# Kernel tuning notes

Measured on AMD Instinct MI355X. Metric: run time of the kernel, lower is better.

The kernel has to match this reference:

```python
import jax, jax.numpy as jnp
import numpy as np

# Hyperparameters (from init_kwargs)
N = 100000      # num_nodes
T = 4           # num_edge_type
E = 400000      # edges per type
C = 2           # num_channels
L = 2           # num_layers
W_IN = 128      # input feature dim
D = 64          # node_dim (w_out)
NUM_CLASS = 16
BETA = 0.5
M = 10000       # number of target nodes


def setup_inputs() -> dict:
    key = jax.random.key(0)
    ks = jax.random.split(key, 10)
    glorot = np.sqrt(6.0 / (W_IN + D))
    glorot1 = np.sqrt(6.0 / (C * D + D))
    glorot2 = np.sqrt(6.0 / (D + NUM_CLASS))
    return {
        "X": jax.random.normal(ks[0], (N, W_IN), dtype=jnp.float32),
        "edge_value": jax.random.uniform(ks[1], (T, E), dtype=jnp.float32),
        "conv_weights": 0.1 * jax.random.normal(ks[2], (L, C, T), dtype=jnp.float32),
        "Ws": jax.random.uniform(ks[3], (C, W_IN, D), minval=-glorot, maxval=glorot, dtype=jnp.float32),
        "lin1_w": jax.random.uniform(ks[4], (C * D, D), minval=-glorot1, maxval=glorot1, dtype=jnp.float32),
        "lin1_b": jnp.zeros((D,), dtype=jnp.float32),
        "lin_w": jax.random.uniform(ks[5], (D, NUM_CLASS), minval=-glorot2, maxval=glorot2, dtype=jnp.float32),
        "lin_b": jnp.zeros((NUM_CLASS,), dtype=jnp.float32),
        "edge_index": jax.random.randint(ks[6], (T, 2, E), 0, N),
        "target_x": jax.random.randint(ks[7], (M,), 0, N),
    }


def reference(X, edge_value, conv_weights, Ws, lin1_w, lin1_b, lin_w, lin_b,
              edge_index, target_x):
    # Flatten edge types into one big edge list. torch_sparse.coalesce(op='add')
    # followed by torch.sparse.mm is mathematically a duplicate-summing SpMM,
    # i.e. a segment_sum over destination rows.
    rows = edge_index[:, 0, :].reshape(-1)      # [T*E]
    cols = edge_index[:, 1, :].reshape(-1)      # [T*E]
    vals = edge_value.reshape(-1)               # [T*E]
    type_id = jnp.repeat(jnp.arange(T), E)      # [T*E] edge-type id (constant)

    # Per-channel input projections: X_ = X @ Ws[c]  -> [C, N, D]
    X_ = jnp.einsum('nf,cfd->cnd', X, Ws)
    H = X_

    for l in range(L):
        # FastGTConv: softmax over edge types per channel
        filt = jax.nn.softmax(conv_weights[l], axis=1)   # [C, T]
        newH = []
        for c in range(C):
            v = vals * filt[c, type_id]                  # [T*E] mixed edge weights
            msgs = v[:, None] * H[c][cols]               # gather + scale: [T*E, D]
            newH.append(jax.ops.segment_sum(msgs, rows, num_segments=N))
        H = jnp.stack(newH)                              # [C, N, D]

    # FastGTN tail: relu(beta*X_ + (1-beta)*H), concat channels, linear1
    Hc = jax.nn.relu(BETA * X_ + (1.0 - BETA) * H)       # [C, N, D]
    Hcat = jnp.transpose(Hc, (1, 0, 2)).reshape(N, C * D)
    H_ = Hcat @ lin1_w + lin1_b                          # [N, D]

    # FastGTNs head: logits at target nodes
    return H_[target_x] @ lin_w + lin_b                  # [M, NUM_CLASS]
```

## Files before the change

### kernel.cpp

```cpp
#include <hip/hip_runtime.h>

#define N_NODES   100000
#define T_TYPES   4
#define E_EDGES   400000
#define E4        100000
#define G_TOT     400000
#define C_CH      2
#define W_INF     128
#define DD        64
#define NUM_CLASS 16
#define BETA      0.5f
#define M_TGT     10000

#define NBKT      391
#define BROWS     256
#define BPAD      4864
#define QPAD      1216
#define CHUNK_G   512
#define NPART_BLK 782
#define PROJ_BLK  1563

static const size_t PLANE2 = (size_t)N_NODES * DD;

typedef __attribute__((ext_vector_type(8))) short short8x;
typedef __attribute__((ext_vector_type(4))) float f32x4;

__device__ __forceinline__ unsigned bf16rne(float x) {
    unsigned u = __float_as_uint(x);
    return (u + 0x7FFFu + ((u >> 16) & 1u)) >> 16;
}
__device__ __forceinline__ unsigned packbf(float a, float b) {
    return bf16rne(a) | (bf16rne(b) << 16);
}
__device__ __forceinline__ float bflo(unsigned u) { return __uint_as_float(u << 16); }
__device__ __forceinline__ float bfhi(unsigned u) { return __uint_as_float(u & 0xFFFF0000u); }

__device__ __forceinline__ void load_filter(const float* cw, int layer,
                                            float* f0, float* f1) {
    float m0 = -1e30f, m1 = -1e30f;
    #pragma unroll
    for (int t = 0; t < T_TYPES; ++t) {
        f0[t] = cw[layer * C_CH * T_TYPES + t];
        f1[t] = cw[layer * C_CH * T_TYPES + T_TYPES + t];
        m0 = fmaxf(m0, f0[t]); m1 = fmaxf(m1, f1[t]);
    }
    float s0 = 0.f, s1 = 0.f;
    #pragma unroll
    for (int t = 0; t < T_TYPES; ++t) {
        f0[t] = __expf(f0[t] - m0); s0 += f0[t];
        f1[t] = __expf(f1[t] - m1); s1 += f1[t];
    }
    #pragma unroll
    for (int t = 0; t < T_TYPES; ++t) { f0[t] /= s0; f1[t] /= s1; }
}

__global__ void prep_kernel(const float* __restrict__ Ws,
                            unsigned short* __restrict__ Wsb,
                            int* __restrict__ cursor) {
    int b = blockIdx.x;
    int tid = threadIdx.x;
    if (b < 64) {
        int idx = b * 256 + tid;
        int c   = idx >> 13;
        int rem = idx & 8191;
        int d   = rem >> 7;
        int k   = rem & 127;
        Wsb[idx] = (unsigned short)bf16rne(Ws[c * (W_INF * DD) + k * DD + d]);
    } else {
        int idx = (b - 64) * 256 + tid;
        if (idx < NBKT) cursor[idx] = idx * BPAD;
    }
}

__global__ __launch_bounds__(256) void build_proj_kernel(
        const int* __restrict__ edge_index,
        const float* __restrict__ edge_value,
        const float* __restrict__ cw,
        int* __restrict__ cursor,
        int2* __restrict__ edata2,
        const float* __restrict__ X,
        const unsigned short* __restrict__ Wsb,
        unsigned* __restrict__ Xp16) {
    __shared__ int cnt[392];
    __shared__ int lbase[392];
    __shared__ int gbase[392];
    __shared__ int2 le[2048];
    __shared__ unsigned short lbk[2048];
    int tid = threadIdx.x;

    if (blockIdx.x < NPART_BLK) {
        int p = blockIdx.x;
        for (int j = tid; j < NBKT; j += 256) cnt[j] = 0;
        __syncthreads();

        float f0[T_TYPES], f1[T_TYPES];
        load_filter(cw, 0, f0, f1);

        int px[8], pv[8], rk[8], bk[8];
        int ne = 0;
        #pragma unroll
        for (int g = 0; g < 2; ++g) {
            int idx = p * CHUNK_G + g * 256 + tid;
            if (idx < G_TOT) {
                int t = idx / E4, r = idx - t * E4;
                const int* bptr = edge_index + (size_t)t * 2 * E_EDGES;
                int4   rw = ((const int4*)bptr)[r];
                int4   cl = ((const int4*)(bptr + E_EDGES))[r];
                float4 vv = ((const float4*)(edge_value + (size_t)t * E_EDGES))[r];
                int tb = t << 17;
                int   rr[4] = {rw.x, rw.y, rw.z, rw.w};
                int   cc[4] = {cl.x, cl.y, cl.z, cl.w};
                float vf[4] = {vv.x, vv.y, vv.z, vv.w};
                #pragma unroll
                for (int k = 0; k < 4; ++k) {
                    int b = rr[k] >> 8;
                    px[ne] = cc[k] | tb | ((rr[k] & 255) << 19);
                    pv[ne] = __float_as_int(vf[k]);
                    bk[ne] = b;
                    rk[ne] = atomicAdd(&cnt[b], 1);
                    ++ne;
                }
            }
        }
        __syncthreads();
        if (tid < 64) {
            int c[7]; int s = 0;
            #pragma unroll
            for (int k = 0; k < 7; ++k) {
                int idx = tid * 7 + k;
                c[k] = (idx < NBKT) ? cnt[idx] : 0;
                s += c[k];
            }
            int inc = s;
            #pragma unroll
            for (int off = 1; off < 64; off <<= 1) {
                int v = __shfl_up(inc, off);
                if (tid >= off) inc += v;
            }
            int base = inc - s;
            #pragma unroll
            for (int k = 0; k < 7; ++k) {
                int idx = tid * 7 + k;
                if (idx < NBKT) lbase[idx] = base;
                base += c[k];
            }
        }
        __syncthreads();
        #pragma unroll
        for (int k = 0; k < 8; ++k) {
            if (k < ne) {
                int slot = lbase[bk[k]] + rk[k];
                le[slot]  = make_int2(px[k], pv[k]);
                lbk[slot] = (unsigned short)bk[k];
            }
        }
        __syncthreads();
        for (int j = tid; j < NBKT; j += 256)
            gbase[j] = cnt[j] ? atomicAdd(&cursor[j], cnt[j]) : 0;
        __syncthreads();
        int ngrp = min(CHUNK_G, G_TOT - p * CHUNK_G);
        int nloc = 4 * ngrp;
        for (int j = tid; j < nloc; j += 256) {
            int b = lbk[j];
            int2 e = le[j];
            int t = (e.x >> 17) & 3;
            float v = __int_as_float(e.y);
            edata2[gbase[b] + (j - lbase[b])] =
                make_int2(e.x, (int)packbf(v * f0[t], v * f1[t]));
        }
    } else {
        int row0 = (blockIdx.x - NPART_BLK) * 64;
        int wave = tid >> 6, lane = tid & 63;
        int m = lane & 15, q = lane >> 4;
        int arow = row0 + wave * 16 + m;
        const float4* X4 = (const float4*)X;
        union { short8x s; uint4 u; } A[4];
        bool valid = arow < N_NODES;
        #pragma unroll
        for (int ks = 0; ks < 4; ++ks) {
            float4 va = make_float4(0.f, 0.f, 0.f, 0.f), vb = va;
            if (valid) {
                va = X4[(size_t)arow * 32 + ks * 8 + q * 2];
                vb = X4[(size_t)arow * 32 + ks * 8 + q * 2 + 1];
            }
            A[ks].u = make_uint4(packbf(va.x, va.y), packbf(va.z, va.w),
                                 packbf(vb.x, vb.y), packbf(vb.z, vb.w));
        }

        #pragma unroll
        for (int ct = 0; ct < 4; ++ct) {
            f32x4 acc0 = {0.f, 0.f, 0.f, 0.f};
            f32x4 acc1 = {0.f, 0.f, 0.f, 0.f};
            #pragma unroll
            for (int ks = 0; ks < 4; ++ks) {
                short8x B0 = *(const short8x*)(Wsb + (ct * 16 + m) * 128 + ks * 32 + q * 8);
                short8x B1 = *(const short8x*)(Wsb + 8192 + (ct * 16 + m) * 128 + ks * 32 + q * 8);
                acc0 = __builtin_amdgcn_mfma_f32_16x16x32_bf16(A[ks].s, B0, acc0, 0, 0, 0);
                acc1 = __builtin_amdgcn_mfma_f32_16x16x32_bf16(A[ks].s, B1, acc1, 0, 0, 0);
            }
            #pragma unroll
            for (int r = 0; r < 4; ++r) {
                int row = row0 + wave * 16 + q * 4 + r;
                if (row < N_NODES)
                    Xp16[(size_t)row * DD + ct * 16 + m] = packbf(acc0[r], acc1[r]);
            }
        }
    }
}

__device__ __forceinline__ void qfma(const uint4 h, unsigned wp,
                                     float4& a, float4& b) {
    float w0 = bflo(wp), w1 = bfhi(wp);
    a.x = fmaf(w0, bflo(h.x), a.x);
    a.y = fmaf(w1, bfhi(h.x), a.y);
    a.z = fmaf(w0, bflo(h.y), a.z);
    a.w = fmaf(w1, bfhi(h.y), a.w);
    b.x = fmaf(w0, bflo(h.z), b.x);
    b.y = fmaf(w1, bfhi(h.z), b.y);
    b.z = fmaf(w0, bflo(h.w), b.z);
    b.w = fmaf(w1, bfhi(h.w), b.w);
}

__device__ __forceinline__ void qreduce(float4& a, float4& b) {
    a.x += __shfl_xor(a.x, 16); a.y += __shfl_xor(a.y, 16);
    a.z += __shfl_xor(a.z, 16); a.w += __shfl_xor(a.w, 16);
    b.x += __shfl_xor(b.x, 16); b.y += __shfl_xor(b.y, 16);
    b.z += __shfl_xor(b.z, 16); b.w += __shfl_xor(b.w, 16);
    a.x += __shfl_xor(a.x, 32); a.y += __shfl_xor(a.y, 32);
    a.z += __shfl_xor(a.z, 32); a.w += __shfl_xor(a.w, 32);
    b.x += __shfl_xor(b.x, 32); b.y += __shfl_xor(b.y, 32);
    b.z += __shfl_xor(b.z, 32); b.w += __shfl_xor(b.w, 32);
}

__device__ __forceinline__ int row_beg(const int* offs, int row) {
    return ((row & 63) == 0) ? (row >> 6) * QPAD : offs[row - 1];
}

__global__ __launch_bounds__(256) void sortgather_kernel(
        const int* __restrict__ cursor,
        const int2* __restrict__ edata2,
        int2* __restrict__ edataS,
        int* __restrict__ offs,
        const unsigned* __restrict__ Hin16,
        unsigned* __restrict__ Hout16) {
    __shared__ int rcnt[64];
    __shared__ int rbase[64];
    __shared__ int rcur[64];
    __shared__ int nq;
    __shared__ int2 ls[QPAD];
    __shared__ unsigned short sidx[QPAD];
    int b = blockIdx.x % 392;
    int q = blockIdx.x / 392;
    if (b >= NBKT) return;
    int tid = threadIdx.x;
    int bb  = b * BPAD;
    int cnt = cursor[b] - bb;

    if (tid < 64) rcnt[tid] = 0;
    if (tid == 0) nq = 0;
    __syncthreads();
    for (int j = tid; j < cnt; j += 256) {
        int2 e = edata2[bb + j];
        int rt = (e.x >> 19) & 255;
        if ((rt >> 6) == q) {
            int pos = atomicAdd(&nq, 1);
            if (pos < QPAD) {
                ls[pos] = e;
                atomicAdd(&rcnt[rt & 63], 1);
            }
        }
    }
    __syncthreads();
    int nl = min(nq, QPAD);
    if (tid < 64) {
        int c = rcnt[tid];
        int inc = c;
        #pragma unroll
        for (int off = 1; off < 64; off <<= 1) {
            int v = __shfl_up(inc, off);
            if (tid >= off) inc += v;
        }
        rbase[tid] = inc - c;
        rcur[tid]  = inc - c;
    }
    __syncthreads();
    for (int j = tid; j < nl; j += 256) {
        int lr = (ls[j].x >> 19) & 63;
        int pos = atomicAdd(&rcur[lr], 1);
        sidx[pos] = (unsigned short)j;
    }
    __syncthreads();

    int s  = b * 4 + q;
    int sb = s * QPAD;
    for (int i = tid; i < nl; i += 256)
        edataS[sb + i] = ls[sidx[i]];
    int row0 = s * 64;
    if (tid < 64 && row0 + tid < N_NODES)
        offs[row0 + tid] = sb + rbase[tid] + rcnt[tid];

    int wv = tid >> 6, lane = tid & 63;
    int s16 = lane & 15, sub = lane >> 4;
    const uint4* hp = (const uint4*)Hin16;
    #pragma unroll 1
    for (int r16 = 0; r16 < 16; ++r16) {
        int lr = wv * 16 + r16;
        int row = row0 + lr;
        int beg = rbase[lr];
        int end = beg + rcnt[lr];
        float4 a  = make_float4(0.f, 0.f, 0.f, 0.f);
        float4 b4 = make_float4(0.f, 0.f, 0.f, 0.f);
        int i = beg + sub;
        for (; i + 4 < end; i += 8) {
            int2 e0 = ls[sidx[i]];
            int2 e1 = ls[sidx[i + 4]];
            uint4 h0 = hp[(size_t)(e0.x & 0x1FFFF) * 16 + s16];
            uint4 h1 = hp[(size_t)(e1.x & 0x1FFFF) * 16 + s16];
            qfma(h0, (unsigned)e0.y, a, b4);
            qfma(h1, (unsigned)e1.y, a, b4);
        }
        if (i < end) {
            int2 e = ls[sidx[i]];
            uint4 h = hp[(size_t)(e.x & 0x1FFFF) * 16 + s16];
            qfma(h, (unsigned)e.y, a, b4);
        }
        qreduce(a, b4);
        if (sub == 0 && row < N_NODES)
            ((uint4*)Hout16)[(size_t)row * 16 + s16] =
                make_uint4(packbf(a.x, a.y), packbf(a.z, a.w),
                           packbf(b4.x, b4.y), packbf(b4.z, b4.w));
    }
}

__global__ __launch_bounds__(256) void tgt_tail_kernel(const unsigned* __restrict__ Hin16,
                                                       const unsigned* __restrict__ Xp16,
                                                       const int* __restrict__ offs,
                                                       const int2* __restrict__ edataS,
                                                       const float* __restrict__ cw,
                                                       const int* __restrict__ tgt,
                                                       const float* __restrict__ lin1_w,
                                                       const float* __restrict__ lin1_b,
                                                       const float* __restrict__ lin_w,
                                                       const float* __restrict__ lin_b,
                                                       float* __restrict__ out) {
    __shared__ float hc[4][W_INF];
    __shared__ float hmid[4][DD];

    int tid = threadIdx.x;

    float f0a[T_TYPES], f1a[T_TYPES], f0b[T_TYPES], f1b[T_TYPES];
    load_filter(cw, 0, f0a, f1a);
    load_filter(cw, 1, f0b, f1b);
    float r0[T_TYPES], r1[T_TYPES];
    #pragma unroll
    for (int t = 0; t < T_TYPES; ++t) { r0[t] = f0b[t] / f0a[t]; r1[t] = f1b[t] / f1a[t]; }

    int w = tid >> 6, lane = tid & 63;
    int s16 = lane & 15, sub = lane >> 4;
    int m = blockIdx.x * 4 + w;
    int row = tgt[m];
    int beg = row_beg(offs, row);
    int end = offs[row];
    const uint4* hp = (const uint4*)Hin16;
    float4 a = make_float4(0.f, 0.f, 0.f, 0.f);
    float4 b = make_float4(0.f, 0.f, 0.f, 0.f);
    for (int i = beg + sub; i < end; i += 4) {
        int2 e = edataS[i];
        int t = (e.x >> 17) & 3;
        uint4 h = hp[(size_t)(e.x & 0x1FFFF) * 16 + s16];
        unsigned wp = (unsigned)e.y;
        float w0 = bflo(wp) * r0[t], w1 = bfhi(wp) * r1[t];
        a.x = fmaf(w0, bflo(h.x), a.x);
        a.y = fmaf(w1, bfhi(h.x), a.y);
        a.z = fmaf(w0, bflo(h.y), a.z);
        a.w = fmaf(w1, bfhi(h.y), a.w);
        b.x = fmaf(w0, bflo(h.z), b.x);
        b.y = fmaf(w1, bfhi(h.z), b.y);
        b.z = fmaf(w0, bflo(h.w), b.z);
        b.w = fmaf(w1, bfhi(h.w), b.w);
    }
    qreduce(a, b);

    if (sub == 0) {
        uint4 xu = ((const uint4*)Xp16)[(size_t)row * 16 + s16];
        int d0 = 4 * s16;
        hc[w][d0 + 0]      = fmaxf(BETA * bflo(xu.x) + (1.f - BETA) * a.x, 0.f);
        hc[w][DD + d0 + 0] = fmaxf(BETA * bfhi(xu.x) + (1.f - BETA) * a.y, 0.f);
        hc[w][d0 + 1]      = fmaxf(BETA * bflo(xu.y) + (1.f - BETA) * a.z, 0.f);
        hc[w][DD + d0 + 1] = fmaxf(BETA * bfhi(xu.y) + (1.f - BETA) * a.w, 0.f);
        hc[w][d0 + 2]      = fmaxf(BETA * bflo(xu.z) + (1.f - BETA) * b.x, 0.f);
        hc[w][DD + d0 + 2] = fmaxf(BETA * bfhi(xu.z) + (1.f - BETA) * b.y, 0.f);
        hc[w][d0 + 3]      = fmaxf(BETA * bflo(xu.w) + (1.f - BETA) * b.z, 0.f);
        hc[w][DD + d0 + 3] = fmaxf(BETA * bfhi(xu.w) + (1.f - BETA) * b.w, 0.f);
    }
    __syncthreads();

    float a1 = lin1_b[lane];
    #pragma unroll 8
    for (int k = 0; k < W_INF; ++k)
        a1 = fmaf(hc[w][k], lin1_w[k * DD + lane], a1);
    hmid[w][lane] = a1;
    __syncthreads();

    if (lane < NUM_CLASS) {
        float o = lin_b[lane];
        #pragma unroll 8
        for (int k = 0; k < DD; ++k)
            o = fmaf(hmid[w][k], lin_w[k * NUM_CLASS + lane], o);
        out[(size_t)m * NUM_CLASS + lane] = o;
    }
}

extern "C" void kernel_launch(void* const* d_in, const int* in_sizes, int n_in,
                              void* d_out, int out_size, void* d_ws, size_t ws_size,
                              hipStream_t stream) {
    const float* X            = (const float*)d_in[0];
    const float* edge_value   = (const float*)d_in[1];
    const float* conv_weights = (const float*)d_in[2];
    const float* Ws           = (const float*)d_in[3];
    const float* lin1_w       = (const float*)d_in[4];
    const float* lin1_b       = (const float*)d_in[5];
    const float* lin_w        = (const float*)d_in[6];
    const float* lin_b        = (const float*)d_in[7];
    const int*   edge_index   = (const int*)d_in[8];
    const int*   target_x     = (const int*)d_in[9];
    float* out = (float*)d_out;

    unsigned*       Xp16 = (unsigned*)d_ws;
    unsigned*       H116 = Xp16 + PLANE2;
    unsigned short* Wsb  = (unsigned short*)(H116 + PLANE2);
    int*            offs = (int*)(Wsb + C_CH * W_INF * DD);
    int*            cursor = offs + N_NODES;
    int2*           edata2 = (int2*)(cursor + 512);
    int2*           edataS = edata2 + (size_t)NBKT * BPAD;

    prep_kernel<<<66, 256, 0, stream>>>(Ws, Wsb, cursor);
    build_proj_kernel<<<NPART_BLK + PROJ_BLK, 256, 0, stream>>>(
        edge_index, edge_value, conv_weights, cursor, edata2, X, Wsb, Xp16);
    sortgather_kernel<<<4 * 392, 256, 0, stream>>>(cursor, edata2, edataS, offs,
                                                   Xp16, H116);
    tgt_tail_kernel<<<M_TGT / 4, 256, 0, stream>>>(H116, Xp16, offs, edataS,
                                                   conv_weights, target_x,
                                                   lin1_w, lin1_b, lin_w, lin_b, out);
}
```

Before: 254.5 us.

## Split sort-gather into 32-row sub-buckets with one quarter-wave per row

```diff
diff --git a/kernel.cpp b/kernel.cpp
--- a/kernel.cpp
+++ b/kernel.cpp
@@ -15,7 +15,7 @@
 #define NBKT      391
 #define BROWS     256
 #define BPAD      4864
-#define QPAD      1216
+#define QPAD      672
 #define CHUNK_G   512
 #define NPART_BLK 782
 #define PROJ_BLK  1563
@@ -233,7 +233,7 @@
 }
 
 __device__ __forceinline__ int row_beg(const int* offs, int row) {
-    return ((row & 63) == 0) ? (row >> 6) * QPAD : offs[row - 1];
+    return ((row & 31) == 0) ? (row >> 5) * QPAD : offs[row - 1];
 }
 
 __global__ __launch_bounds__(256) void sortgather_kernel(
@@ -243,40 +243,40 @@
         int* __restrict__ offs,
         const unsigned* __restrict__ Hin16,
         unsigned* __restrict__ Hout16) {
-    __shared__ int rcnt[64];
-    __shared__ int rbase[64];
-    __shared__ int rcur[64];
+    __shared__ int rcnt[32];
+    __shared__ int rbase[32];
+    __shared__ int rcur[32];
     __shared__ int nq;
     __shared__ int2 ls[QPAD];
-    __shared__ unsigned short sidx[QPAD];
+    __shared__ int2 ls2[QPAD];
     int b = blockIdx.x % 392;
-    int q = blockIdx.x / 392;
+    int o = blockIdx.x / 392;
     if (b >= NBKT) return;
     int tid = threadIdx.x;
     int bb  = b * BPAD;
     int cnt = cursor[b] - bb;
 
-    if (tid < 64) rcnt[tid] = 0;
+    if (tid < 32) rcnt[tid] = 0;
     if (tid == 0) nq = 0;
     __syncthreads();
     for (int j = tid; j < cnt; j += 256) {
         int2 e = edata2[bb + j];
         int rt = (e.x >> 19) & 255;
-        if ((rt >> 6) == q) {
+        if ((rt >> 5) == o) {
             int pos = atomicAdd(&nq, 1);
             if (pos < QPAD) {
                 ls[pos] = e;
-                atomicAdd(&rcnt[rt & 63], 1);
+                atomicAdd(&rcnt[rt & 31], 1);
             }
         }
     }
     __syncthreads();
     int nl = min(nq, QPAD);
-    if (tid < 64) {
+    if (tid < 32) {
         int c = rcnt[tid];
         int inc = c;
         #pragma unroll
-        for (int off = 1; off < 64; off <<= 1) {
+        for (int off = 1; off < 32; off <<= 1) {
             int v = __shfl_up(inc, off);
             if (tid >= off) inc += v;
         }
@@ -285,47 +285,63 @@
     }
     __syncthreads();
     for (int j = tid; j < nl; j += 256) {
-        int lr = (ls[j].x >> 19) & 63;
+        int2 e = ls[j];
+        int lr = (e.x >> 19) & 31;
         int pos = atomicAdd(&rcur[lr], 1);
-        sidx[pos] = (unsigned short)j;
-    }
-    __syncthreads();
-
-    int s  = b * 4 + q;
+        ls2[pos] = e;
+    }
+    __syncthreads();
+
+    int s  = b * 8 + o;
     int sb = s * QPAD;
     for (int i = tid; i < nl; i += 256)
-        edataS[sb + i] = ls[sidx[i]];
-    int row0 = s * 64;
-    if (tid < 64 && row0 + tid < N_NODES)
+        edataS[sb + i] = ls2[i];
+    int row0 = s * 32;
+    if (tid < 32 && row0 + tid < N_NODES)
         offs[row0 + tid] = sb + rbase[tid] + rcnt[tid];
+    __syncthreads();
 
     int wv = tid >> 6, lane = tid & 63;
-    int s16 = lane & 15, sub = lane >> 4;
+    int s16 = lane & 15, qd = lane >> 4;
     const uint4* hp = (const uint4*)Hin16;
-    #pragma unroll 1
-    for (int r16 = 0; r16 < 16; ++r16) {
-        int lr = wv * 16 + r16;
+    #pragma unroll
+    for (int rr = 0; rr < 2; ++rr) {
+        int lr  = wv * 8 + rr * 4 + qd;
         int row = row0 + lr;
         int beg = rbase[lr];
         int end = beg + rcnt[lr];
         float4 a  = make_float4(0.f, 0.f, 0.f, 0.f);
         float4 b4 = make_float4(0.f, 0.f, 0.f, 0.f);
-        int i = beg + sub;
-        for (; i + 4 < end; i += 8) {
-            int2 e0 = ls[sidx[i]];
-            int2 e1 = ls[sidx[i + 4]];
+        int i = beg;
+        for (; i + 3 < end; i += 4) {
+            int2 e0 = ls2[i];
+            int2 e1 = ls2[i + 1];
+            int2 e2 = ls2[i + 2];
+            int2 e3 = ls2[i + 3];
+            uint4 h0 = hp[(size_t)(e0.x & 0x1FFFF) * 16 + s16];
+            uint4 h1 = hp[(size_t)(e1.x & 0x1FFFF) * 16 + s16];
+            uint4 h2 = hp[(size_t)(e2.x & 0x1FFFF) * 16 + s16];
+            uint4 h3 = hp[(size_t)(e3.x & 0x1FFFF) * 16 + s16];
+            qfma(h0, (unsigned)e0.y, a, b4);
+            qfma(h1, (unsigned)e1.y, a, b4);
+            qfma(h2, (unsigned)e2.y, a, b4);
+            qfma(h3, (unsigned)e3.y, a, b4);
+        }
+        if (i + 1 < end) {
+            int2 e0 = ls2[i];
+            int2 e1 = ls2[i + 1];
             uint4 h0 = hp[(size_t)(e0.x & 0x1FFFF) * 16 + s16];
             uint4 h1 = hp[(size_t)(e1.x & 0x1FFFF) * 16 + s16];
             qfma(h0, (unsigned)e0.y, a, b4);
             qfma(h1, (unsigned)e1.y, a, b4);
+            i += 2;
         }
         if (i < end) {
-            int2 e = ls[sidx[i]];
+            int2 e = ls2[i];
             uint4 h = hp[(size_t)(e.x & 0x1FFFF) * 16 + s16];
             qfma(h, (unsigned)e.y, a, b4);
         }
-        qreduce(a, b4);
-        if (sub == 0 && row < N_NODES)
+        if (row < N_NODES)
             ((uint4*)Hout16)[(size_t)row * 16 + s16] =
                 make_uint4(packbf(a.x, a.y), packbf(a.z, a.w),
                            packbf(b4.x, b4.y), packbf(b4.z, b4.w));
@@ -437,7 +453,7 @@
     prep_kernel<<<66, 256, 0, stream>>>(Ws, Wsb, cursor);
     build_proj_kernel<<<NPART_BLK + PROJ_BLK, 256, 0, stream>>>(
         edge_index, edge_value, conv_weights, cursor, edata2, X, Wsb, Xp16);
-    sortgather_kernel<<<4 * 392, 256, 0, stream>>>(cursor, edata2, edataS, offs,
+    sortgather_kernel<<<8 * 392, 256, 0, stream>>>(cursor, edata2, edataS, offs,
                                                    Xp16, H116);
     tgt_tail_kernel<<<M_TGT / 4, 256, 0, stream>>>(H116, Xp16, offs, edataS,
                                                    conv_weights, target_x,
```

New measurement: 253.2 us. About the same (-0.5%).
